# Kernel optimization log

Measured on AMD Instinct MI355X. Metric: run time of the kernel, lower is better.

The kernel has to match this reference:

```python
import jax, jax.numpy as jnp
import numpy as np

NUM_OPS = 8
D = 1024
B = 8192


def setup_inputs() -> dict:
    key = jax.random.key(0)
    k1, k2, k3, k4 = jax.random.split(key, 4)
    x = jax.random.normal(k1, (B, D), dtype=jnp.float32)
    logits = 0.001 * jax.random.normal(k2, (NUM_OPS,), dtype=jnp.float32)
    Ws = jax.random.normal(k3, (NUM_OPS, D, D), dtype=jnp.float32) * (1.0 / np.sqrt(D))
    bs = jax.random.normal(k4, (NUM_OPS, D), dtype=jnp.float32) * 0.01
    return {"x": x, "logits": logits, "Ws": Ws, "bs": bs, "num_on_samples": 2}


def reference(x, logits, Ws, bs, num_on_samples):
    # non_stochastic_call: top-k op selection by architecture logits,
    # dispatch x to the selected ops, sum-combine the results.
    _, top_k_ids = jax.lax.top_k(logits, num_on_samples)  # [k]
    W_sel = jnp.take(Ws, top_k_ids, axis=0)  # [k, D, D]
    b_sel = jnp.take(bs, top_k_ids, axis=0)  # [k, D]
    # each op is Dense(D->D) + relu: [k, B, D]
    op_results = jax.nn.relu(jnp.einsum('bd,kde->kbe', x, W_sel) + b_sel[:, None, :])
    return jnp.sum(op_results, axis=0)  # [B, D]
```

## Files before the change

### kernel.cpp

```cpp
#include <hip/hip_runtime.h>
#include <hip/hip_bf16.h>

#define NUM_OPS 8
#define D 1024
#define B_ROWS 8192

typedef unsigned short ushort_t;
typedef __attribute__((ext_vector_type(8))) short bf16x8;
typedef __attribute__((ext_vector_type(4))) float f32x4;
typedef __attribute__((ext_vector_type(4))) float float4v;
typedef __attribute__((ext_vector_type(8))) unsigned short ushort8;

__device__ __forceinline__ unsigned short f2bf(float f) {
    union { float f; unsigned int u; } v; v.f = f;
    unsigned int u = v.u;
    unsigned int lsb = (u >> 16) & 1u;
    u += 0x7fffu + lsb;
    return (unsigned short)(u >> 16);
}

__device__ __forceinline__ void top2(const float* __restrict__ logits, int& i0, int& i1) {
    float best = -__builtin_inff(); i0 = 0;
    for (int i = 0; i < NUM_OPS; ++i) { float v = logits[i]; if (v > best) { best = v; i0 = i; } }
    float best2 = -__builtin_inff(); i1 = 0;
    for (int i = 0; i < NUM_OPS; ++i) {
        if (i == i0) continue;
        float v = logits[i]; if (v > best2) { best2 = v; i1 = i; }
    }
}

__global__ void convert_frag_x(const float* __restrict__ x, ushort_t* __restrict__ Af) {
    __shared__ float t[64][65];
    const int b = blockIdx.x;
    const int r = b >> 4, u = b & 15;
    const int tid = threadIdx.x;

    const int row = tid >> 2, c0 = (tid & 3) * 16;
    const float* src = x + (size_t)(r * 64 + row) * D + u * 64 + c0;
    #pragma unroll
    for (int j = 0; j < 4; ++j) {
        float4v v = *(const float4v*)(src + j * 4);
        t[row][c0 + j * 4 + 0] = v[0];
        t[row][c0 + j * 4 + 1] = v[1];
        t[row][c0 + j * 4 + 2] = v[2];
        t[row][c0 + j * 4 + 3] = v[3];
    }
    __syncthreads();

    #pragma unroll
    for (int g2 = 0; g2 < 2; ++g2) {
        const int g = g2 * 256 + tid;
        const int f = g >> 6, lane = g & 63;
        const int kk = f >> 2, m = f & 3;
        const int rr = m * 16 + (lane & 15);
        const int cc = kk * 32 + (lane >> 4) * 8;
        ushort8 o;
        #pragma unroll
        for (int j = 0; j < 8; ++j) o[j] = f2bf(t[rr][cc + j]);
        *(ushort8*)(Af + ((size_t)(r * 16 + u) * 8 + f) * 512 + lane * 8) = o;
    }
}

__global__ void gather_frag_W(const float* __restrict__ Ws,
                              const float* __restrict__ logits,
                              ushort_t* __restrict__ Wf) {
    __shared__ float t[32][33];
    int s0, s1; top2(logits, s0, s1);
    const int b  = blockIdx.x;
    const int nt = b & 31, kt = (b >> 5) & 31, e = b >> 10;
    const int td = kt * 32, te = nt * 32;
    const int tx = threadIdx.x & 31, ty = threadIdx.x >> 5;
    const float* W = Ws + (size_t)(e ? s1 : s0) * D * D;
    #pragma unroll
    for (int r = 0; r < 4; ++r)
        t[ty + 8 * r][tx] = W[(size_t)(td + ty + 8 * r) * D + te + tx];
    __syncthreads();
    const int vid = threadIdx.x;
    if (vid < 128) {
        const int n_l = vid & 31, kg = vid >> 5;
        const int n = te + n_l, k0 = td + kg * 8;
        const int u = k0 >> 6, kk = (k0 >> 5) & 1, lq = (k0 >> 3) & 3;
        const int p = n >> 5, n16 = (n >> 4) & 1, l15 = n & 15;
        const int lane = lq * 16 + l15;
        const int fi = (((e * 32 + p) * 16 + u) * 2 + kk) * 2 + n16;
        ushort8 o;
        #pragma unroll
        for (int j = 0; j < 8; ++j) o[j] = f2bf(t[kg * 8 + j][n_l]);
        *(ushort8*)(Wf + (size_t)fi * 512 + lane * 8) = o;
    }
}

#define SB()    __builtin_amdgcn_sched_barrier(0)
#define PRIO1() __builtin_amdgcn_s_setprio(1)
#define PRIO0() __builtin_amdgcn_s_setprio(0)
#define VMW(N)  do { asm volatile("s_waitcnt vmcnt(" #N ")" ::: "memory"); SB(); } while (0)

#define GLD(dst, off, base, imm)                                               \
    asm volatile("global_load_dwordx4 %0, %1, %2 offset:" #imm                 \
                 : "=v"(dst) : "v"(off), "s"(base) : "memory")

#define ISSUE(P, u)                                                            \
    do {                                                                       \
        unsigned vA  = aoff + (unsigned)(u) * 8192u;                           \
        unsigned vA2 = vA + 4096u;                                             \
        unsigned vB  = boff + (unsigned)(u) * 4096u;                           \
        unsigned vB2 = vB + 2097152u;                                          \
        GLD(P##a0, vA,  Af, 0);    GLD(P##a1, vA,  Af, 1024);                  \
        GLD(P##a2, vA,  Af, 2048); GLD(P##a3, vA,  Af, 3072);                  \
        GLD(P##a4, vA2, Af, 0);    GLD(P##a5, vA2, Af, 1024);                  \
        GLD(P##a6, vA2, Af, 2048); GLD(P##a7, vA2, Af, 3072);                  \
        GLD(P##b0, vB,  Wf, 0);    GLD(P##b1, vB,  Wf, 1024);                  \
        GLD(P##b2, vB,  Wf, 2048); GLD(P##b3, vB,  Wf, 3072);                  \
        GLD(P##b4, vB2, Wf, 0);    GLD(P##b5, vB2, Wf, 1024);                  \
        GLD(P##b6, vB2, Wf, 2048); GLD(P##b7, vB2, Wf, 3072);                  \
    } while (0)

#define MF(a, b, c) __builtin_amdgcn_mfma_f32_16x16x32_bf16(a, b, c, 0, 0, 0)
#define Q(P, A, B, E, M, N) acc[E][M][N] = MF(P##A, P##B, acc[E][M][N])

#define MFMA_SET(P)                                                            \
    do {                                                                       \
        PRIO1();                                                               \
        Q(P,a0,b0,0,0,0); Q(P,a0,b1,0,0,1); Q(P,a0,b4,1,0,0); Q(P,a0,b5,1,0,1);\
        Q(P,a1,b0,0,1,0); Q(P,a1,b1,0,1,1); Q(P,a1,b4,1,1,0); Q(P,a1,b5,1,1,1);\
        Q(P,a2,b0,0,2,0); Q(P,a2,b1,0,2,1); Q(P,a2,b4,1,2,0); Q(P,a2,b5,1,2,1);\
        Q(P,a3,b0,0,3,0); Q(P,a3,b1,0,3,1); Q(P,a3,b4,1,3,0); Q(P,a3,b5,1,3,1);\
        Q(P,a4,b2,0,0,0); Q(P,a4,b3,0,0,1); Q(P,a4,b6,1,0,0); Q(P,a4,b7,1,0,1);\
        Q(P,a5,b2,0,1,0); Q(P,a5,b3,0,1,1); Q(P,a5,b6,1,1,0); Q(P,a5,b7,1,1,1);\
        Q(P,a6,b2,0,2,0); Q(P,a6,b3,0,2,1); Q(P,a6,b6,1,2,0); Q(P,a6,b7,1,2,1);\
        Q(P,a7,b2,0,3,0); Q(P,a7,b3,0,3,1); Q(P,a7,b6,1,3,0); Q(P,a7,b7,1,3,1);\
        PRIO0();                                                               \
    } while (0)

__global__ __launch_bounds__(256, 2)
void gemm_frag(const ushort_t* __restrict__ Af, const ushort_t* __restrict__ Wf,
               const float* __restrict__ bs, const float* __restrict__ logits,
               float* __restrict__ out) {
    const int tid  = threadIdx.x;
    const int wv   = tid >> 6;
    const int lane = tid & 63;
    const int l15  = lane & 15, lq = lane >> 4;

    const int bid = blockIdx.x;
    const int rp  = (bid & 7) * 8 + ((bid >> 3) & 7);
    const int r   = rp * 2 + (wv & 1);
    const int p   = (bid >> 6) * 2 + (wv >> 1);

    const unsigned aoff = (unsigned)r * 131072u + (unsigned)lane * 16u;
    const unsigned boff = (unsigned)p * 65536u  + (unsigned)lane * 16u;

    f32x4 acc[2][4][2] = {};

    bf16x8 Xa0, Xa1, Xa2, Xa3, Xa4, Xa5, Xa6, Xa7;
    bf16x8 Xb0, Xb1, Xb2, Xb3, Xb4, Xb5, Xb6, Xb7;
    bf16x8 Ya0, Ya1, Ya2, Ya3, Ya4, Ya5, Ya6, Ya7;
    bf16x8 Yb0, Yb1, Yb2, Yb3, Yb4, Yb5, Yb6, Yb7;

    ISSUE(X, 0); SB();
    ISSUE(Y, 1); SB();

    #pragma unroll 1
    for (int u = 0; u < 14; u += 2) {
        VMW(16);
        MFMA_SET(X); SB();
        ISSUE(X, u + 2); SB();
        VMW(16);
        MFMA_SET(Y); SB();
        ISSUE(Y, u + 3); SB();
    }
    VMW(16);
    MFMA_SET(X); SB();
    VMW(0);
    MFMA_SET(Y); SB();

    int i0, i1; top2(logits, i0, i1);
    #pragma unroll
    for (int n16 = 0; n16 < 2; ++n16) {
        const int col = p * 32 + n16 * 16 + l15;
        const float b0 = bs[i0 * D + col];
        const float b1 = bs[i1 * D + col];
        #pragma unroll
        for (int m = 0; m < 4; ++m) {
            const int rbase = r * 64 + m * 16 + lq * 4;
            #pragma unroll
            for (int i = 0; i < 4; ++i) {
                float v0 = acc[0][m][n16][i] + b0; v0 = v0 > 0.f ? v0 : 0.f;
                float v1 = acc[1][m][n16][i] + b1; v1 = v1 > 0.f ? v1 : 0.f;
                out[(size_t)(rbase + i) * D + col] = v0 + v1;
            }
        }
    }
}

extern "C" void kernel_launch(void* const* d_in, const int* in_sizes, int n_in,
                              void* d_out, int out_size, void* d_ws, size_t ws_size,
                              hipStream_t stream) {
    const float* x      = (const float*)d_in[0];
    const float* logits = (const float*)d_in[1];
    const float* Ws     = (const float*)d_in[2];
    const float* bs     = (const float*)d_in[3];
    float* out = (float*)d_out;

    char* ws = (char*)d_ws;
    ushort_t* Af = (ushort_t*)ws;
    ushort_t* Wf = (ushort_t*)(ws + (size_t)B_ROWS * D * 2);

    convert_frag_x<<<128 * 16, 256, 0, stream>>>(x, Af);
    gather_frag_W<<<2 * 32 * 32, 256, 0, stream>>>(Ws, logits, Wf);

    gemm_frag<<<1024, 256, 0, stream>>>(Af, Wf, bs, logits, out);
}
```

Measured before the change: 55.81 us.

## Merge prep kernels and split GEMM load/MFMA pipeline into half-stages

```diff
diff --git a/kernel.cpp b/kernel.cpp
--- a/kernel.cpp
+++ b/kernel.cpp
@@ -29,64 +29,64 @@
     }
 }
 
-__global__ void convert_frag_x(const float* __restrict__ x, ushort_t* __restrict__ Af) {
-    __shared__ float t[64][65];
-    const int b = blockIdx.x;
-    const int r = b >> 4, u = b & 15;
+__global__ void prep_kernel(const float* __restrict__ x,
+                            const float* __restrict__ Ws,
+                            const float* __restrict__ logits,
+                            ushort_t* __restrict__ Af,
+                            ushort_t* __restrict__ Wf) {
+    __shared__ __align__(16) float smem[64 * 65];
+    const int bid = blockIdx.x;
     const int tid = threadIdx.x;
 
-    const int row = tid >> 2, c0 = (tid & 3) * 16;
-    const float* src = x + (size_t)(r * 64 + row) * D + u * 64 + c0;
-    #pragma unroll
-    for (int j = 0; j < 4; ++j) {
-        float4v v = *(const float4v*)(src + j * 4);
-        t[row][c0 + j * 4 + 0] = v[0];
-        t[row][c0 + j * 4 + 1] = v[1];
-        t[row][c0 + j * 4 + 2] = v[2];
-        t[row][c0 + j * 4 + 3] = v[3];
-    }
-    __syncthreads();
-
-    #pragma unroll
-    for (int g2 = 0; g2 < 2; ++g2) {
-        const int g = g2 * 256 + tid;
-        const int f = g >> 6, lane = g & 63;
-        const int kk = f >> 2, m = f & 3;
-        const int rr = m * 16 + (lane & 15);
-        const int cc = kk * 32 + (lane >> 4) * 8;
-        ushort8 o;
-        #pragma unroll
-        for (int j = 0; j < 8; ++j) o[j] = f2bf(t[rr][cc + j]);
-        *(ushort8*)(Af + ((size_t)(r * 16 + u) * 8 + f) * 512 + lane * 8) = o;
-    }
-}
-
-__global__ void gather_frag_W(const float* __restrict__ Ws,
-                              const float* __restrict__ logits,
-                              ushort_t* __restrict__ Wf) {
-    __shared__ float t[32][33];
-    int s0, s1; top2(logits, s0, s1);
-    const int b  = blockIdx.x;
-    const int nt = b & 31, kt = (b >> 5) & 31, e = b >> 10;
-    const int td = kt * 32, te = nt * 32;
-    const int tx = threadIdx.x & 31, ty = threadIdx.x >> 5;
-    const float* W = Ws + (size_t)(e ? s1 : s0) * D * D;
-    #pragma unroll
-    for (int r = 0; r < 4; ++r)
-        t[ty + 8 * r][tx] = W[(size_t)(td + ty + 8 * r) * D + te + tx];
-    __syncthreads();
-    const int vid = threadIdx.x;
-    if (vid < 128) {
-        const int n_l = vid & 31, kg = vid >> 5;
-        const int n = te + n_l, k0 = td + kg * 8;
-        const int u = k0 >> 6, kk = (k0 >> 5) & 1, lq = (k0 >> 3) & 3;
-        const int p = n >> 5, n16 = (n >> 4) & 1, l15 = n & 15;
-        const int lane = lq * 16 + l15;
-        const int fi = (((e * 32 + p) * 16 + u) * 2 + kk) * 2 + n16;
-        ushort8 o;
-        #pragma unroll
-        for (int j = 0; j < 8; ++j) o[j] = f2bf(t[kg * 8 + j][n_l]);
-        *(ushort8*)(Wf + (size_t)fi * 512 + lane * 8) = o;
+    if (bid < 2048) {
+        const int b = bid;
+        const int r = b >> 4, u = b & 15;
+        const int row = tid >> 2, c0 = (tid & 3) * 16;
+        const float* src = x + (size_t)(r * 64 + row) * D + u * 64 + c0;
+        #pragma unroll
+        for (int j = 0; j < 4; ++j) {
+            float4v v = *(const float4v*)(src + j * 4);
+            smem[row * 65 + c0 + j * 4 + 0] = v[0];
+            smem[row * 65 + c0 + j * 4 + 1] = v[1];
+            smem[row * 65 + c0 + j * 4 + 2] = v[2];
+            smem[row * 65 + c0 + j * 4 + 3] = v[3];
+        }
+        __syncthreads();
+        #pragma unroll
+        for (int g2 = 0; g2 < 2; ++g2) {
+            const int g = g2 * 256 + tid;
+            const int f = g >> 6, lane = g & 63;
+            const int kk = f >> 2, m = f & 3;
+            const int rr = m * 16 + (lane & 15);
+            const int cc = kk * 32 + (lane >> 4) * 8;
+            ushort8 o;
+            #pragma unroll
+            for (int j = 0; j < 8; ++j) o[j] = f2bf(smem[rr * 65 + cc + j]);
+            *(ushort8*)(Af + ((size_t)(r * 16 + u) * 8 + f) * 512 + lane * 8) = o;
+        }
+    } else {
+        int s0, s1; top2(logits, s0, s1);
+        const int b  = bid - 2048;
+        const int nt = b & 31, kt = (b >> 5) & 31, e = b >> 10;
+        const int td = kt * 32, te = nt * 32;
+        const int tx = tid & 31, ty = tid >> 5;
+        const float* W = Ws + (size_t)(e ? s1 : s0) * D * D;
+        #pragma unroll
+        for (int r = 0; r < 4; ++r)
+            smem[(ty + 8 * r) * 33 + tx] = W[(size_t)(td + ty + 8 * r) * D + te + tx];
+        __syncthreads();
+        if (tid < 128) {
+            const int n_l = tid & 31, kg = tid >> 5;
+            const int n = te + n_l, k0 = td + kg * 8;
+            const int u = k0 >> 6, kk = (k0 >> 5) & 1, lq = (k0 >> 3) & 3;
+            const int p = n >> 5, n16 = (n >> 4) & 1, l15 = n & 15;
+            const int lane = lq * 16 + l15;
+            const int fi = (((e * 32 + p) * 16 + u) * 2 + kk) * 2 + n16;
+            ushort8 o;
+            #pragma unroll
+            for (int j = 0; j < 8; ++j) o[j] = f2bf(smem[(kg * 8 + j) * 33 + n_l]);
+            *(ushort8*)(Wf + (size_t)fi * 512 + lane * 8) = o;
+        }
     }
 }
 
@@ -99,32 +99,44 @@
     asm volatile("global_load_dwordx4 %0, %1, %2 offset:" #imm                 \
                  : "=v"(dst) : "v"(off), "s"(base) : "memory")
 
-#define ISSUE(P, u)                                                            \
-    do {                                                                       \
-        unsigned vA  = aoff + (unsigned)(u) * 8192u;                           \
-        unsigned vA2 = vA + 4096u;                                             \
-        unsigned vB  = boff + (unsigned)(u) * 4096u;                           \
+#define ISSUE_H0(P, u)                                                         \
+    do {                                                                       \
+        unsigned vA = aoff + (unsigned)(u) * 8192u;                            \
+        unsigned vB = boff + (unsigned)(u) * 4096u;                            \
         unsigned vB2 = vB + 2097152u;                                          \
-        GLD(P##a0, vA,  Af, 0);    GLD(P##a1, vA,  Af, 1024);                  \
-        GLD(P##a2, vA,  Af, 2048); GLD(P##a3, vA,  Af, 3072);                  \
+        GLD(P##a0, vA, Af, 0);    GLD(P##a1, vA, Af, 1024);                    \
+        GLD(P##a2, vA, Af, 2048); GLD(P##a3, vA, Af, 3072);                    \
+        GLD(P##b0, vB, Wf, 0);    GLD(P##b1, vB, Wf, 1024);                    \
+        GLD(P##b4, vB2, Wf, 0);   GLD(P##b5, vB2, Wf, 1024);                   \
+    } while (0)
+
+#define ISSUE_H1(P, u)                                                         \
+    do {                                                                       \
+        unsigned vA2 = aoff + (unsigned)(u) * 8192u + 4096u;                   \
+        unsigned vB = boff + (unsigned)(u) * 4096u;                            \
+        unsigned vB2 = vB + 2097152u;                                          \
         GLD(P##a4, vA2, Af, 0);    GLD(P##a5, vA2, Af, 1024);                  \
         GLD(P##a6, vA2, Af, 2048); GLD(P##a7, vA2, Af, 3072);                  \
-        GLD(P##b0, vB,  Wf, 0);    GLD(P##b1, vB,  Wf, 1024);                  \
-        GLD(P##b2, vB,  Wf, 2048); GLD(P##b3, vB,  Wf, 3072);                  \
-        GLD(P##b4, vB2, Wf, 0);    GLD(P##b5, vB2, Wf, 1024);                  \
+        GLD(P##b2, vB, Wf, 2048);  GLD(P##b3, vB, Wf, 3072);                   \
         GLD(P##b6, vB2, Wf, 2048); GLD(P##b7, vB2, Wf, 3072);                  \
     } while (0)
 
 #define MF(a, b, c) __builtin_amdgcn_mfma_f32_16x16x32_bf16(a, b, c, 0, 0, 0)
 #define Q(P, A, B, E, M, N) acc[E][M][N] = MF(P##A, P##B, acc[E][M][N])
 
-#define MFMA_SET(P)                                                            \
+#define MFMA_H0(P)                                                             \
     do {                                                                       \
         PRIO1();                                                               \
         Q(P,a0,b0,0,0,0); Q(P,a0,b1,0,0,1); Q(P,a0,b4,1,0,0); Q(P,a0,b5,1,0,1);\
         Q(P,a1,b0,0,1,0); Q(P,a1,b1,0,1,1); Q(P,a1,b4,1,1,0); Q(P,a1,b5,1,1,1);\
         Q(P,a2,b0,0,2,0); Q(P,a2,b1,0,2,1); Q(P,a2,b4,1,2,0); Q(P,a2,b5,1,2,1);\
         Q(P,a3,b0,0,3,0); Q(P,a3,b1,0,3,1); Q(P,a3,b4,1,3,0); Q(P,a3,b5,1,3,1);\
+        PRIO0();                                                               \
+    } while (0)
+
+#define MFMA_H1(P)                                                             \
+    do {                                                                       \
+        PRIO1();                                                               \
         Q(P,a4,b2,0,0,0); Q(P,a4,b3,0,0,1); Q(P,a4,b6,1,0,0); Q(P,a4,b7,1,0,1);\
         Q(P,a5,b2,0,1,0); Q(P,a5,b3,0,1,1); Q(P,a5,b6,1,1,0); Q(P,a5,b7,1,1,1);\
         Q(P,a6,b2,0,2,0); Q(P,a6,b3,0,2,1); Q(P,a6,b6,1,2,0); Q(P,a6,b7,1,2,1);\
@@ -141,10 +153,8 @@
     const int lane = tid & 63;
     const int l15  = lane & 15, lq = lane >> 4;
 
-    const int bid = blockIdx.x;
-    const int rp  = (bid & 7) * 8 + ((bid >> 3) & 7);
-    const int r   = rp * 2 + (wv & 1);
-    const int p   = (bid >> 6) * 2 + (wv >> 1);
+    const int r = (blockIdx.x & 63) * 2 + (wv & 1);
+    const int p = (blockIdx.x >> 6) * 2 + (wv >> 1);
 
     const unsigned aoff = (unsigned)r * 131072u + (unsigned)lane * 16u;
     const unsigned boff = (unsigned)p * 65536u  + (unsigned)lane * 16u;
@@ -156,22 +166,30 @@
     bf16x8 Ya0, Ya1, Ya2, Ya3, Ya4, Ya5, Ya6, Ya7;
     bf16x8 Yb0, Yb1, Yb2, Yb3, Yb4, Yb5, Yb6, Yb7;
 
-    ISSUE(X, 0); SB();
-    ISSUE(Y, 1); SB();
+    ISSUE_H0(X, 0); SB();
+    ISSUE_H1(X, 0); SB();
+    ISSUE_H0(Y, 1); SB();
+    ISSUE_H1(Y, 1); SB();
 
     #pragma unroll 1
     for (int u = 0; u < 14; u += 2) {
-        VMW(16);
-        MFMA_SET(X); SB();
-        ISSUE(X, u + 2); SB();
-        VMW(16);
-        MFMA_SET(Y); SB();
-        ISSUE(Y, u + 3); SB();
-    }
-    VMW(16);
-    MFMA_SET(X); SB();
-    VMW(0);
-    MFMA_SET(Y); SB();
+        VMW(24);
+        MFMA_H0(X); SB();
+        ISSUE_H0(X, u + 2); SB();
+        VMW(24);
+        MFMA_H1(X); SB();
+        ISSUE_H1(X, u + 2); SB();
+        VMW(24);
+        MFMA_H0(Y); SB();
+        ISSUE_H0(Y, u + 3); SB();
+        VMW(24);
+        MFMA_H1(Y); SB();
+        ISSUE_H1(Y, u + 3); SB();
+    }
+    VMW(24); MFMA_H0(X); SB();
+    VMW(16); MFMA_H1(X); SB();
+    VMW(8);  MFMA_H0(Y); SB();
+    VMW(0);  MFMA_H1(Y); SB();
 
     int i0, i1; top2(logits, i0, i1);
     #pragma unroll
@@ -205,8 +223,6 @@
     ushort_t* Af = (ushort_t*)ws;
     ushort_t* Wf = (ushort_t*)(ws + (size_t)B_ROWS * D * 2);
 
-    convert_frag_x<<<128 * 16, 256, 0, stream>>>(x, Af);
-    gather_frag_W<<<2 * 32 * 32, 256, 0, stream>>>(Ws, logits, Wf);
-
+    prep_kernel<<<4096, 256, 0, stream>>>(x, Ws, logits, Af, Wf);
     gemm_frag<<<1024, 256, 0, stream>>>(Af, Wf, bs, logits, out);
 }
```

After: 54.44 us. 2.4% less time.
